# Kernel tuning notes

Hardware: AMD Instinct MI355X
Metric: run time of the kernel (lower is better)

## Reference

```python
import jax, jax.numpy as jnp
import numpy as np

B, D, NCLS = 65536, 784, 10

def sparse_layer(x, idx, w, b):
    # x: [B, D]; idx: [Dout, k] int; w: [Dout, k]; b: [Dout]
    # out[b, n] = sum_j x[b, idx[n, j]] * w[n, j] + b[n]
    g = x[:, idx]                      # [B, Dout, k] gather
    return jnp.einsum('bnk,nk->bn', g, w) + b

def setup_inputs() -> dict:
    key = jax.random.key(0)
    ks = jax.random.split(key, 12)
    def rn(k, shape, scale):
        return jax.random.normal(k, shape, dtype=jnp.float32) * scale
    return {
        'x': rn(ks[0], (B, D), 1.0),
        'idx1': jax.random.randint(ks[1], (D, 2), 0, D, dtype=jnp.int32),
        'w1': rn(ks[2], (D, 2), 0.5),
        'b1': rn(ks[3], (D,), 0.1),
        'idx2': jax.random.randint(ks[4], (D, 4), 0, D, dtype=jnp.int32),
        'w2': rn(ks[5], (D, 4), 0.4),
        'b2': rn(ks[6], (D,), 0.1),
        'idx3': jax.random.randint(ks[7], (D, 8), 0, D, dtype=jnp.int32),
        'w3': rn(ks[8], (D, 8), 0.3),
        'b3': rn(ks[9], (D,), 0.1),
        'fc_w': rn(ks[10], (NCLS, D), 0.05),
        'fc_b': rn(ks[11], (NCLS,), 0.05),
    }

def reference(x, idx1, w1, b1, idx2, w2, b2, idx3, w3, b3, fc_w, fc_b):
    h = jax.nn.gelu(sparse_layer(x, idx1, w1, b1), approximate=False)
    h = jax.nn.gelu(sparse_layer(h, idx2, w2, b2), approximate=False)
    h = jax.nn.gelu(sparse_layer(h, idx3, w3, b3), approximate=False)
    logits = h @ fc_w.T + fc_b          # [B, 10]
    return jax.nn.softmax(logits, axis=-1)
```

## Files before the change

### kernel.cpp

```cpp
#include <hip/hip_runtime.h>

#define D_     784
#define ROWS   8
#define NCLS   10
#define BLOCK  640
#define NB     (65536 / ROWS)
#define PL     (D_ * 4)
#define TAIL   (D_ - BLOCK)

__device__ __forceinline__ float gelu_f(float x) {
    float x2    = x * x;
    float inner = fmaf(0.044715f * x, x2, x);
    float e     = exp2f(2.3022082f * inner);
    float r     = __builtin_amdgcn_rcpf(e + 1.0f);
    return fmaf(-x, r, x);
}

__device__ __forceinline__ float4 gelu4(const float4& a) {
    return make_float4(gelu_f(a.x), gelu_f(a.y), gelu_f(a.z), gelu_f(a.w));
}

__device__ __forceinline__ void fma4(float4& a, const float4& h4, float wk) {
    a.x = fmaf(h4.x, wk, a.x);
    a.y = fmaf(h4.y, wk, a.y);
    a.z = fmaf(h4.z, wk, a.z);
    a.w = fmaf(h4.w, wk, a.w);
}

template <int K>
__device__ __forceinline__ void loadIdxW(const int* __restrict__ idx,
                                         const float* __restrict__ w,
                                         int n, int* jc, float* wc) {
    if constexpr (K == 2) {
        int2   j = *(const int2*)(idx + n * 2);
        float2 v = *(const float2*)(w + n * 2);
        jc[0] = j.x; jc[1] = j.y; wc[0] = v.x; wc[1] = v.y;
    } else if constexpr (K == 4) {
        int4   j = *(const int4*)(idx + n * 4);
        float4 v = *(const float4*)(w + n * 4);
        jc[0] = j.x; jc[1] = j.y; jc[2] = j.z; jc[3] = j.w;
        wc[0] = v.x; wc[1] = v.y; wc[2] = v.z; wc[3] = v.w;
    } else {
        int4   ja = *(const int4*)(idx + n * 8);
        int4   jb = *(const int4*)(idx + n * 8 + 4);
        float4 va = *(const float4*)(w + n * 8);
        float4 vb = *(const float4*)(w + n * 8 + 4);
        jc[0] = ja.x; jc[1] = ja.y; jc[2] = ja.z; jc[3] = ja.w;
        jc[4] = jb.x; jc[5] = jb.y; jc[6] = jb.z; jc[7] = jb.w;
        wc[0] = va.x; wc[1] = va.y; wc[2] = va.z; wc[3] = va.w;
        wc[4] = vb.x; wc[5] = vb.y; wc[6] = vb.z; wc[7] = vb.w;
    }
}

template <int K>
__device__ __forceinline__ void layer_one(const float* __restrict__ src,
                                          float* __restrict__ dst,
                                          const int* __restrict__ idx,
                                          const float* __restrict__ w,
                                          const float* __restrict__ bias,
                                          int n) {
    int   jc[K];
    float wc[K];
    loadIdxW<K>(idx, w, n, jc, wc);
    float  bc = bias[n];
    float4 lo = make_float4(bc, bc, bc, bc);
    float4 hi = lo;
#pragma unroll
    for (int k = 0; k < K; ++k) {
        const float* g = src + jc[k] * 4;
        float4 gl = *(const float4*)g;
        float4 gh = *(const float4*)(g + PL);
        fma4(lo, gl, wc[k]);
        fma4(hi, gh, wc[k]);
    }
    *(float4*)(dst + n * 4)      = gelu4(lo);
    *(float4*)(dst + n * 4 + PL) = gelu4(hi);
}

__global__ __launch_bounds__(BLOCK)
void circnn_kernel(const float* __restrict__ x,
                   const int* __restrict__ idx1, const float* __restrict__ w1, const float* __restrict__ b1,
                   const int* __restrict__ idx2, const float* __restrict__ w2, const float* __restrict__ b2,
                   const int* __restrict__ idx3, const float* __restrict__ w3, const float* __restrict__ b3,
                   const float* __restrict__ fcw, const float* __restrict__ fcb,
                   float* __restrict__ out) {
    __shared__ __align__(16) float bufA[D_ * ROWS];
    __shared__ __align__(16) float bufB[D_ * ROWS];
    __shared__ float logits[ROWS * NCLS];

    const int tid  = threadIdx.x;
    const int row0 = blockIdx.x * ROWS;

    const float* xb = x + (size_t)row0 * D_;
    {
        int n = tid;
        float4 lo, hi;
        lo.x = xb[0 * D_ + n]; lo.y = xb[1 * D_ + n];
        lo.z = xb[2 * D_ + n]; lo.w = xb[3 * D_ + n];
        hi.x = xb[4 * D_ + n]; hi.y = xb[5 * D_ + n];
        hi.z = xb[6 * D_ + n]; hi.w = xb[7 * D_ + n];
        *(float4*)(bufA + n * 4)      = lo;
        *(float4*)(bufA + n * 4 + PL) = hi;
    }
    if (tid < TAIL) {
        int n = BLOCK + tid;
        float4 lo, hi;
        lo.x = xb[0 * D_ + n]; lo.y = xb[1 * D_ + n];
        lo.z = xb[2 * D_ + n]; lo.w = xb[3 * D_ + n];
        hi.x = xb[4 * D_ + n]; hi.y = xb[5 * D_ + n];
        hi.z = xb[6 * D_ + n]; hi.w = xb[7 * D_ + n];
        *(float4*)(bufA + n * 4)      = lo;
        *(float4*)(bufA + n * 4 + PL) = hi;
    }
    __syncthreads();

    layer_one<2>(bufA, bufB, idx1, w1, b1, tid);
    if (tid < TAIL) layer_one<2>(bufA, bufB, idx1, w1, b1, BLOCK + tid);
    __syncthreads();

    layer_one<4>(bufB, bufA, idx2, w2, b2, tid);
    if (tid < TAIL) layer_one<4>(bufB, bufA, idx2, w2, b2, BLOCK + tid);
    __syncthreads();

    layer_one<8>(bufA, bufB, idx3, w3, b3, tid);
    if (tid < TAIL) layer_one<8>(bufA, bufB, idx3, w3, b3, BLOCK + tid);
    __syncthreads();

    float4* part4 = (float4*)bufA;
    if (tid < 128) {
        const int jj = tid >> 1;
        const int qq = tid & 1;
        float4 facc[NCLS];
#pragma unroll
        for (int c = 0; c < NCLS; ++c) facc[c] = make_float4(0.f, 0.f, 0.f, 0.f);
#pragma unroll 1
        for (int i = 0; i < 13; ++i) {
            int n = jj + 64 * i;
            if (n < D_) {
                float4 hv = *(const float4*)(bufB + qq * PL + n * 4);
#pragma unroll
                for (int c = 0; c < NCLS; ++c)
                    fma4(facc[c], hv, fcw[c * D_ + n]);
            }
        }
#pragma unroll
        for (int c = 0; c < NCLS; ++c)
            part4[(jj * 2 + qq) * NCLS + c] = facc[c];
    }
    __syncthreads();

    if (tid < ROWS * NCLS) {
        int r = tid / NCLS, c = tid - r * NCLS;
        int qq = r >> 2, comp = r & 3;
        const float* pf = (const float*)part4;
        float s = fcb[c];
#pragma unroll 4
        for (int jj = 0; jj < 64; ++jj)
            s += pf[((jj * 2 + qq) * NCLS + c) * 4 + comp];
        logits[tid] = s;
    }
    __syncthreads();

    if (tid < ROWS * NCLS) {
        int r = tid / NCLS;
        const float* lg = logits + r * NCLS;
        float m = lg[0];
#pragma unroll
        for (int c = 1; c < NCLS; ++c) m = fmaxf(m, lg[c]);
        float s = 0.f;
#pragma unroll
        for (int c = 0; c < NCLS; ++c) s += __expf(lg[c] - m);
        out[(size_t)row0 * NCLS + tid] = __expf(logits[tid] - m) / s;
    }
}

extern "C" void kernel_launch(void* const* d_in, const int* in_sizes, int n_in,
                              void* d_out, int out_size, void* d_ws, size_t ws_size,
                              hipStream_t stream) {
    const float* x    = (const float*)d_in[0];
    const int*   idx1 = (const int*)d_in[1];
    const float* w1   = (const float*)d_in[2];
    const float* b1   = (const float*)d_in[3];
    const int*   idx2 = (const int*)d_in[4];
    const float* w2   = (const float*)d_in[5];
    const float* b2   = (const float*)d_in[6];
    const int*   idx3 = (const int*)d_in[7];
    const float* w3   = (const float*)d_in[8];
    const float* b3   = (const float*)d_in[9];
    const float* fcw  = (const float*)d_in[10];
    const float* fcb  = (const float*)d_in[11];
    float* out = (float*)d_out;

    circnn_kernel<<<dim3(NB), dim3(BLOCK), 0, stream>>>(
        x, idx1, w1, b1, idx2, w2, b2, idx3, w3, b3, fcw, fcb, out);
}
```

Measured before the change: 462.8 us.

## Process 16 rows per block with 1024 threads, one neuron per thread

Doubles the rows handled per block from 8 to 16 and raises block size to 1024 so each thread owns one neuron without a tail loop. Each idx/weight load is now reused across four float4 row groups, halving per-row index/weight traffic and removing the divergent tail pass. Shared memory doubles to about 100KB per block, which limits occupancy to one block per CU, and 240 threads sit idle during the layers.

```diff
diff --git a/kernel.cpp b/kernel.cpp
--- a/kernel.cpp
+++ b/kernel.cpp
@@ -1,12 +1,11 @@
 #include <hip/hip_runtime.h>
 
 #define D_     784
-#define ROWS   8
+#define ROWS   16
 #define NCLS   10
-#define BLOCK  640
+#define BLOCK  1024
 #define NB     (65536 / ROWS)
 #define PL     (D_ * 4)
-#define TAIL   (D_ - BLOCK)
 
 __device__ __forceinline__ float gelu_f(float x) {
     float x2    = x * x;
@@ -63,18 +62,21 @@
     float wc[K];
     loadIdxW<K>(idx, w, n, jc, wc);
     float  bc = bias[n];
-    float4 lo = make_float4(bc, bc, bc, bc);
-    float4 hi = lo;
+    float4 a0 = make_float4(bc, bc, bc, bc);
+    float4 a1 = a0, a2 = a0, a3 = a0;
 #pragma unroll
     for (int k = 0; k < K; ++k) {
         const float* g = src + jc[k] * 4;
-        float4 gl = *(const float4*)g;
-        float4 gh = *(const float4*)(g + PL);
-        fma4(lo, gl, wc[k]);
-        fma4(hi, gh, wc[k]);
+        fma4(a0, *(const float4*)(g),          wc[k]);
+        fma4(a1, *(const float4*)(g + PL),     wc[k]);
+        fma4(a2, *(const float4*)(g + 2 * PL), wc[k]);
+        fma4(a3, *(const float4*)(g + 3 * PL), wc[k]);
     }
-    *(float4*)(dst + n * 4)      = gelu4(lo);
-    *(float4*)(dst + n * 4 + PL) = gelu4(hi);
+    float* d = dst + n * 4;
+    *(float4*)(d)          = gelu4(a0);
+    *(float4*)(d + PL)     = gelu4(a1);
+    *(float4*)(d + 2 * PL) = gelu4(a2);
+    *(float4*)(d + 3 * PL) = gelu4(a3);
 }
 
 __global__ __launch_bounds__(BLOCK)
@@ -91,45 +93,34 @@
     const int tid  = threadIdx.x;
     const int row0 = blockIdx.x * ROWS;
 
-    const float* xb = x + (size_t)row0 * D_;
-    {
-        int n = tid;
-        float4 lo, hi;
-        lo.x = xb[0 * D_ + n]; lo.y = xb[1 * D_ + n];
-        lo.z = xb[2 * D_ + n]; lo.w = xb[3 * D_ + n];
-        hi.x = xb[4 * D_ + n]; hi.y = xb[5 * D_ + n];
-        hi.z = xb[6 * D_ + n]; hi.w = xb[7 * D_ + n];
-        *(float4*)(bufA + n * 4)      = lo;
-        *(float4*)(bufA + n * 4 + PL) = hi;
-    }
-    if (tid < TAIL) {
-        int n = BLOCK + tid;
-        float4 lo, hi;
-        lo.x = xb[0 * D_ + n]; lo.y = xb[1 * D_ + n];
-        lo.z = xb[2 * D_ + n]; lo.w = xb[3 * D_ + n];
-        hi.x = xb[4 * D_ + n]; hi.y = xb[5 * D_ + n];
-        hi.z = xb[6 * D_ + n]; hi.w = xb[7 * D_ + n];
-        *(float4*)(bufA + n * 4)      = lo;
-        *(float4*)(bufA + n * 4 + PL) = hi;
+    if (tid < D_) {
+        const float* xb = x + (size_t)row0 * D_ + tid;
+        float4 q0, q1, q2, q3;
+        q0.x = xb[ 0 * D_]; q0.y = xb[ 1 * D_]; q0.z = xb[ 2 * D_]; q0.w = xb[ 3 * D_];
+        q1.x = xb[ 4 * D_]; q1.y = xb[ 5 * D_]; q1.z = xb[ 6 * D_]; q1.w = xb[ 7 * D_];
+        q2.x = xb[ 8 * D_]; q2.y = xb[ 9 * D_]; q2.z = xb[10 * D_]; q2.w = xb[11 * D_];
+        q3.x = xb[12 * D_]; q3.y = xb[13 * D_]; q3.z = xb[14 * D_]; q3.w = xb[15 * D_];
+        float* d = bufA + tid * 4;
+        *(float4*)(d)          = q0;
+        *(float4*)(d + PL)     = q1;
+        *(float4*)(d + 2 * PL) = q2;
+        *(float4*)(d + 3 * PL) = q3;
     }
     __syncthreads();
 
-    layer_one<2>(bufA, bufB, idx1, w1, b1, tid);
-    if (tid < TAIL) layer_one<2>(bufA, bufB, idx1, w1, b1, BLOCK + tid);
+    if (tid < D_) layer_one<2>(bufA, bufB, idx1, w1, b1, tid);
     __syncthreads();
 
-    layer_one<4>(bufB, bufA, idx2, w2, b2, tid);
-    if (tid < TAIL) layer_one<4>(bufB, bufA, idx2, w2, b2, BLOCK + tid);
+    if (tid < D_) layer_one<4>(bufB, bufA, idx2, w2, b2, tid);
     __syncthreads();
 
-    layer_one<8>(bufA, bufB, idx3, w3, b3, tid);
-    if (tid < TAIL) layer_one<8>(bufA, bufB, idx3, w3, b3, BLOCK + tid);
+    if (tid < D_) layer_one<8>(bufA, bufB, idx3, w3, b3, tid);
     __syncthreads();
 
     float4* part4 = (float4*)bufA;
-    if (tid < 128) {
-        const int jj = tid >> 1;
-        const int qq = tid & 1;
+    if (tid < 256) {
+        const int jj = tid >> 2;
+        const int qq = tid & 3;
         float4 facc[NCLS];
 #pragma unroll
         for (int c = 0; c < NCLS; ++c) facc[c] = make_float4(0.f, 0.f, 0.f, 0.f);
@@ -145,7 +136,7 @@
         }
 #pragma unroll
         for (int c = 0; c < NCLS; ++c)
-            part4[(jj * 2 + qq) * NCLS + c] = facc[c];
+            part4[(jj * 4 + qq) * NCLS + c] = facc[c];
     }
     __syncthreads();
 
@@ -156,7 +147,7 @@
         float s = fcb[c];
 #pragma unroll 4
         for (int jj = 0; jj < 64; ++jj)
-            s += pf[((jj * 2 + qq) * NCLS + c) * 4 + comp];
+            s += pf[((jj * 4 + qq) * NCLS + c) * 4 + comp];
         logits[tid] = s;
     }
     __syncthreads();
```

New measurement: 462.9 us. No clear change (+0.0%).
